# Performance work log

Measured on AMD Instinct MI355X. Metric: run time of the kernel, lower is better.

Reference implementation:

```python
import jax, jax.numpy as jnp
import numpy as np

B, N, D, H, E = 8, 2048, 128, 256, 524288
EPS = 1e-5

def setup_inputs() -> dict:
    key = jax.random.key(0)
    ks = jax.random.split(key, 16)
    def lin(k, fan_in, shape):
        b = 1.0 / np.sqrt(fan_in)
        return jax.random.uniform(k, shape, jnp.float32, -b, b)
    return {
        'x': jax.random.normal(ks[0], (B, N, 3), jnp.float32),
        'h': jax.random.normal(ks[1], (B, N, D), jnp.float32),
        'edge_indices': jax.random.randint(ks[2], (2, E), 0, B * N, jnp.int64),
        'batch_size': B,
        # filter_net: Linear(1,H) -> SiLU -> Linear(H,D)   (weights stored [in,out])
        'W1': lin(ks[3], 1, (1, H)), 'b1': lin(ks[4], 1, (H,)),
        'W2': lin(ks[5], H, (H, D)), 'b2': lin(ks[6], H, (D,)),
        # update_net: Linear(2D,H) -> LayerNorm(H) -> SiLU -> Linear(H,D)
        'W3': lin(ks[7], 2 * D, (2 * D, H)), 'b3': lin(ks[8], 2 * D, (H,)),
        'gamma': jnp.ones((H,), jnp.float32), 'beta': jnp.zeros((H,), jnp.float32),
        'W4': lin(ks[9], H, (H, D)), 'b4': lin(ks[10], H, (D,)),
    }

def reference(x, h, edge_indices, batch_size, W1, b1, W2, b2, W3, b3, gamma, beta, W4, b4):
    Bn, Nn, Dn = h.shape
    row, col = edge_indices[0], edge_indices[1]
    br, nr = row // Nn, row % Nn
    bc, nc = col // Nn, col % Nn
    x_row = x[br, nr]            # [E,3] gather
    x_col = x[bc, nc]            # [E,3]
    h_col = h[bc, nc]            # [E,D]
    diff = x_row - x_col
    dist = jnp.sqrt(jnp.sum(diff * diff, axis=-1, keepdims=True))  # [E,1]
    # distance-conditioned edge filter MLP
    edge_filters = jax.nn.silu(dist @ W1 + b1) @ W2 + b2           # [E,D]
    messages = h_col * edge_filters                                 # [E,D]
    # scatter-mean into B*N nodes (single-pass sum + count, clamp_min(1))
    n_tot = Bn * Nn
    sums = jax.ops.segment_sum(messages, row, num_segments=n_tot)
    counts = jax.ops.segment_sum(jnp.ones_like(row, dtype=messages.dtype), row, num_segments=n_tot)
    agg = (sums / jnp.maximum(counts, 1.0)[:, None]).reshape(Bn, Nn, Dn)
    # update MLP with LayerNorm
    u = jnp.concatenate([h, agg], axis=-1) @ W3 + b3               # [B,N,H]
    mu = jnp.mean(u, axis=-1, keepdims=True)
    var = jnp.mean((u - mu) ** 2, axis=-1, keepdims=True)
    un = (u - mu) * jax.lax.rsqrt(var + EPS) * gamma + beta
    return jax.nn.silu(un) @ W4 + b4                                # [B,N,D]
```

## Files before the change

### kernel.cpp

```cpp
#include <hip/hip_runtime.h>
#include <hip/hip_fp16.h>
#include <math.h>

#define BN_NODES 16384
#define DIM 128
#define HID 256
#define TK 4096
#define TRANGE 32.0f
#define TSTEP (TRANGE / (float)TK)
#define TINV  ((float)TK / TRANGE)
#define LN_EPS 1e-5f
#define EPB 4096
#define NBINS 1024
#define CAPB 768

typedef _Float16 f16x8 __attribute__((ext_vector_type(8)));
typedef __attribute__((ext_vector_type(4))) float f32x4;
typedef __attribute__((ext_vector_type(2))) float floatx2;
typedef __attribute__((ext_vector_type(8))) unsigned short ushort8v;

__device__ __forceinline__ unsigned short f2h(float f) {
    _Float16 h = (_Float16)f;
    return *(unsigned short*)&h;
}
__device__ __forceinline__ __half2 u2h2(unsigned int u) {
    union { unsigned int u; __half2 h; } c; c.u = u; return c.h;
}

__device__ __forceinline__ void edge_acc(unsigned int rec, int dd,
        const unsigned char* __restrict__ xq,
        const unsigned short* __restrict__ Tb, float& a0, float& a1) {
    int c = (int)((rec >> 12) & 0x3FFFu);
    int k = (int)(rec & 0xFFFu);
    unsigned short hq = *(const unsigned short*)&xq[c * DIM + dd];
    unsigned int tv = *(const unsigned int*)&Tb[k * DIM + dd];
    floatx2 hf = __builtin_amdgcn_cvt_pk_f32_fp8((int)hq, false);
    __half2 th = u2h2(tv);
    a0 = fmaf(hf[0], __low2float(th), a0);
    a1 = fmaf(hf[1], __high2float(th), a1);
}

__device__ __forceinline__ void node_tail(const unsigned int* lrec, int from, int to,
        int dd, const unsigned char* __restrict__ xq,
        const unsigned short* __restrict__ Tb, float& a0, float& a1) {
    int i = from;
    for (; i + 4 <= to; i += 4) {
        unsigned int e0 = lrec[i], e1 = lrec[i + 1], e2 = lrec[i + 2], e3 = lrec[i + 3];
        edge_acc(e0, dd, xq, Tb, a0, a1);
        edge_acc(e1, dd, xq, Tb, a0, a1);
        edge_acc(e2, dd, xq, Tb, a0, a1);
        edge_acc(e3, dd, xq, Tb, a0, a1);
    }
    for (; i < to; ++i) edge_acc(lrec[i], dd, xq, Tb, a0, a1);
}

__global__ __launch_bounds__(256) void prep_kernel(
        const float* __restrict__ W1, const float* __restrict__ b1,
        const float* __restrict__ W2, const float* __restrict__ b2,
        const float* __restrict__ W3, const float* __restrict__ W4,
        const float* __restrict__ h, const int* __restrict__ ei,
        const float* __restrict__ x,
        unsigned short* __restrict__ Tb, unsigned short* __restrict__ w3t,
        unsigned short* __restrict__ w4t, unsigned short* __restrict__ xh,
        unsigned char* __restrict__ xq, int* __restrict__ bin_cursor,
        unsigned int* __restrict__ staging, int nE) {
    __shared__ float smem[8 * 256 + 8 * 128];
    int bid = blockIdx.x, t = threadIdx.x;
    if (bid < 512) {
        float* a    = smem;
        float* part = smem + 8 * 256;
        int k0 = bid * 8;
        float w1 = W1[t], bb = b1[t];
#pragma unroll
        for (int k = 0; k < 8; ++k) {
            float dist = ((float)(k0 + k) + 0.5f) * TSTEP;
            float z = dist * w1 + bb;
            a[k * 256 + t] = z / (1.0f + expf(-z));
        }
        __syncthreads();
        int hg = t >> 7, d = t & 127;
        float acc[8] = {0.f,0.f,0.f,0.f,0.f,0.f,0.f,0.f};
        for (int hh = 0; hh < 128; ++hh) {
            int hidx = hg * 128 + hh;
            float w = W2[hidx * DIM + d];
#pragma unroll
            for (int k = 0; k < 8; ++k) acc[k] += a[k * 256 + hidx] * w;
        }
        if (hg == 1) {
#pragma unroll
            for (int k = 0; k < 8; ++k) part[k * 128 + d] = acc[k];
        }
        __syncthreads();
        if (hg == 0) {
            float bd = b2[d];
#pragma unroll
            for (int k = 0; k < 8; ++k)
                Tb[(k0 + k) * DIM + d] = f2h(acc[k] + part[k * 128 + d] + bd);
        }
    } else if (bid < 576) {
        float* s = smem;
        int tid = bid - 512, tr = tid >> 3, tc = tid & 7;
        int lr = t >> 5, lc = t & 31;
#pragma unroll
        for (int rep = 0; rep < 4; ++rep) {
            int k = tr * 32 + rep * 8 + lr, n = tc * 32 + lc;
            s[lc * 33 + rep * 8 + lr] = W3[k * 256 + n];
        }
        __syncthreads();
#pragma unroll
        for (int rep = 0; rep < 4; ++rep) {
            int n = tc * 32 + rep * 8 + lr, k = tr * 32 + lc;
            w3t[n * 256 + k] = f2h(s[(rep * 8 + lr) * 33 + lc]);
        }
    } else if (bid < 608) {
        float* s = smem;
        int tid = bid - 576, tr = tid >> 2, tc = tid & 3;
        int lr = t >> 5, lc = t & 31;
#pragma unroll
        for (int rep = 0; rep < 4; ++rep) {
            int k = tr * 32 + rep * 8 + lr, n = tc * 32 + lc;
            s[lc * 33 + rep * 8 + lr] = W4[k * 128 + n];
        }
        __syncthreads();
#pragma unroll
        for (int rep = 0; rep < 4; ++rep) {
            int n = tc * 32 + rep * 8 + lr, k = tr * 32 + lc;
            w4t[n * 256 + k] = f2h(s[(rep * 8 + lr) * 33 + lc]);
        }
    } else if (bid < 1632) {
        int i0 = (bid - 608) * 2048 + t * 8;
        float4 v0 = *(const float4*)&h[i0];
        float4 v1 = *(const float4*)&h[i0 + 4];
        ushort8v o;
        o[0] = f2h(v0.x); o[1] = f2h(v0.y); o[2] = f2h(v0.z); o[3] = f2h(v0.w);
        o[4] = f2h(v1.x); o[5] = f2h(v1.y); o[6] = f2h(v1.z); o[7] = f2h(v1.w);
        *(ushort8v*)&xh[i0] = o;
        unsigned int q0 = 0, q1 = 0;
        q0 = __builtin_amdgcn_cvt_pk_fp8_f32(v0.x, v0.y, q0, false);
        q0 = __builtin_amdgcn_cvt_pk_fp8_f32(v0.z, v0.w, q0, true);
        q1 = __builtin_amdgcn_cvt_pk_fp8_f32(v1.x, v1.y, q1, false);
        q1 = __builtin_amdgcn_cvt_pk_fp8_f32(v1.z, v1.w, q1, true);
        uint2 qq; qq.x = q0; qq.y = q1;
        *(uint2*)&xq[i0] = qq;
    } else {
        __shared__ int cnt[NBINS];
        __shared__ int pre[NBINS];
        __shared__ int gba[NBINS];
        __shared__ int sc[256];
        __shared__ unsigned int rec[EPB];
        int e0 = (bid - 1632) * EPB;
        int m = min(EPB, nE - e0);
        if (m < 0) m = 0;
#pragma unroll
        for (int j = 0; j < 4; ++j) cnt[j * 256 + t] = 0;
        __syncthreads();
        unsigned int code[16];
        int rk[16], bn[16];
#pragma unroll
        for (int j = 0; j < 16; ++j) {
            int idx = j * 256 + t;
            rk[j] = -1; bn[j] = 0; code[j] = 0;
            if (idx < m) {
                int e = e0 + idx;
                int r = ei[e], c = ei[nE + e];
                code[j] = ((unsigned int)r << 14) | (unsigned int)c;
                bn[j] = r >> 4;
                rk[j] = atomicAdd(&cnt[bn[j]], 1);
            }
        }
        __syncthreads();
        int c4[4], s4 = 0;
#pragma unroll
        for (int j = 0; j < 4; ++j) { c4[j] = cnt[t * 4 + j]; s4 += c4[j]; }
        sc[t] = s4;
        __syncthreads();
        for (int off = 1; off < 256; off <<= 1) {
            int v = (t >= off) ? sc[t - off] : 0;
            __syncthreads();
            sc[t] += v;
            __syncthreads();
        }
        int run = sc[t] - s4;
#pragma unroll
        for (int j = 0; j < 4; ++j) {
            int b = t * 4 + j;
            pre[b] = run; run += c4[j];
            gba[b] = atomicAdd(&bin_cursor[b], c4[j]);
        }
        __syncthreads();
#pragma unroll
        for (int j = 0; j < 16; ++j)
            if (rk[j] >= 0) rec[pre[bn[j]] + rk[j]] = code[j];
        __syncthreads();
        for (int i = t; i < m; i += 256) {
            unsigned int cd = rec[i];
            int b = (int)(cd >> 18);
            int r = (int)(cd >> 14);
            int c = (int)(cd & 0x3FFFu);
            float dx = x[r * 3 + 0] - x[c * 3 + 0];
            float dy = x[r * 3 + 1] - x[c * 3 + 1];
            float dz = x[r * 3 + 2] - x[c * 3 + 2];
            float u = sqrtf(dx * dx + dy * dy + dz * dz) * TINV;
            int k = min((int)u, TK - 1);
            unsigned int o = ((unsigned int)(r & 15) << 26)
                           | ((unsigned int)c << 12) | (unsigned int)k;
            int off = gba[b] + (i - pre[b]);
            if (off < CAPB) staging[b * CAPB + off] = o;
        }
    }
}

__global__ __launch_bounds__(512, 8) void mega_kernel(
        const unsigned int* __restrict__ staging, const int* __restrict__ bin_cursor,
        const unsigned short* __restrict__ Tb, const unsigned char* __restrict__ xq,
        const unsigned short* __restrict__ xh, const unsigned short* __restrict__ w3t,
        const float* __restrict__ b3, const float* __restrict__ gamma,
        const float* __restrict__ beta, const unsigned short* __restrict__ w4t,
        const float* __restrict__ b4, float* __restrict__ out) {
    __shared__ unsigned int lrec[CAPB];
    __shared__ int cnt16[16];
    __shared__ int pref[17];
    __shared__ int cur[16];
    __shared__ __align__(16) unsigned short aggh[16][136];
    __shared__ __align__(16) unsigned short a_lds[16][264];
    __shared__ float part_s[8][16], part_q[8][16];
    __shared__ float tot_mu[16], tot_rs[16];

    int t = threadIdx.x;
    int bin = blockIdx.x;
    int n0 = bin * 16;
    if (t < 16) cnt16[t] = 0;
    __syncthreads();
    int total = min(bin_cursor[bin], CAPB);
    long base = (long)bin * CAPB;

    unsigned int sr0 = 0, sr1 = 0;
    int have0 = (t < total), have1 = (t + 512 < total);
    if (have0) { sr0 = staging[base + t];       atomicAdd(&cnt16[sr0 >> 26], 1); }
    if (have1) { sr1 = staging[base + t + 512]; atomicAdd(&cnt16[sr1 >> 26], 1); }
    __syncthreads();
    if (t < 16) {
        int c = cnt16[t];
        int s = c;
#pragma unroll
        for (int off = 1; off < 16; off <<= 1) {
            int v = __shfl_up(s, off, 16);
            if (t >= off) s += v;
        }
        pref[t + 1] = s;
        cur[t] = s - c;
        if (t == 0) pref[0] = 0;
    }
    __syncthreads();

    if (have0) { int pos = atomicAdd(&cur[sr0 >> 26], 1); lrec[pos] = sr0; }
    if (have1) { int pos = atomicAdd(&cur[sr1 >> 26], 1); lrec[pos] = sr1; }
    __syncthreads();

    int wid = t >> 6, lane = t & 63, dd = lane * 2;

    {
        int j0 = wid * 2, j1 = j0 + 1;
        int off0 = pref[j0], len0 = pref[j0 + 1] - off0;
        int off1 = pref[j1], len1 = pref[j1 + 1] - off1;
        float a0x = 0.f, a0y = 0.f, a1x = 0.f, a1y = 0.f;
        int minl = min(len0, len1);
        int i = 0;
        for (; i + 8 <= minl; i += 8) {
#pragma unroll
            for (int u = 0; u < 8; ++u) {
                edge_acc(lrec[off0 + i + u], dd, xq, Tb, a0x, a0y);
                edge_acc(lrec[off1 + i + u], dd, xq, Tb, a1x, a1y);
            }
        }
        node_tail(lrec, off0 + i, off0 + len0, dd, xq, Tb, a0x, a0y);
        node_tail(lrec, off1 + i, off1 + len1, dd, xq, Tb, a1x, a1y);
        float inv0 = 1.0f / (float)max(len0, 1);
        float inv1 = 1.0f / (float)max(len1, 1);
        unsigned int p0 = (unsigned int)f2h(a0x * inv0) | ((unsigned int)f2h(a0y * inv0) << 16);
        unsigned int p1 = (unsigned int)f2h(a1x * inv1) | ((unsigned int)f2h(a1y * inv1) << 16);
        *(unsigned int*)&aggh[j0][dd] = p0;
        *(unsigned int*)&aggh[j1][dd] = p1;
    }
    __syncthreads();

    int wv = wid, q = lane >> 4, l15 = lane & 15;
    f32x4 acc[2];
    acc[0] = (f32x4){0.f, 0.f, 0.f, 0.f};
    acc[1] = (f32x4){0.f, 0.f, 0.f, 0.f};
    for (int kc = 0; kc < 8; ++kc) {
        f16x8 a;
        if (kc < 4) a = *(const f16x8*)&xh[(n0 + l15) * DIM + kc * 32 + q * 8];
        else        a = *(const f16x8*)&aggh[l15][(kc - 4) * 32 + q * 8];
#pragma unroll
        for (int nt = 0; nt < 2; ++nt) {
            f16x8 b = *(const f16x8*)&w3t[(wv * 32 + nt * 16 + l15) * 256 + kc * 32 + q * 8];
            acc[nt] = __builtin_amdgcn_mfma_f32_16x16x32_f16(a, b, acc[nt], 0, 0, 0);
        }
    }

    float b3v[2], gv[2], bvv[2];
#pragma unroll
    for (int nt = 0; nt < 2; ++nt) {
        int col = wv * 32 + nt * 16 + l15;
        b3v[nt] = b3[col]; gv[nt] = gamma[col]; bvv[nt] = beta[col];
    }
    {
        float s_[4], q_[4];
#pragma unroll
        for (int reg = 0; reg < 4; ++reg) {
            float su = 0.f, sq = 0.f;
#pragma unroll
            for (int nt = 0; nt < 2; ++nt) {
                float v = acc[nt][reg] + b3v[nt];
                acc[nt][reg] = v;
                su += v; sq += v * v;
            }
            s_[reg] = su; q_[reg] = sq;
        }
#pragma unroll
        for (int off = 1; off < 16; off <<= 1) {
#pragma unroll
            for (int reg = 0; reg < 4; ++reg) {
                s_[reg] += __shfl_xor(s_[reg], off, 64);
                q_[reg] += __shfl_xor(q_[reg], off, 64);
            }
        }
        if (l15 == 0) {
#pragma unroll
            for (int reg = 0; reg < 4; ++reg) {
                int r = q * 4 + reg;
                part_s[wv][r] = s_[reg];
                part_q[wv][r] = q_[reg];
            }
        }
    }
    __syncthreads();
    if (t < 16) {
        float st = 0.f, qt = 0.f;
#pragma unroll
        for (int w = 0; w < 8; ++w) { st += part_s[w][t]; qt += part_q[w][t]; }
        float mu = st * (1.0f / 256.0f);
        float var = qt * (1.0f / 256.0f) - mu * mu;
        tot_mu[t] = mu;
        tot_rs[t] = rsqrtf(var + LN_EPS);
    }
    __syncthreads();

#pragma unroll
    for (int reg = 0; reg < 4; ++reg) {
        int r = q * 4 + reg;
        float mu = tot_mu[r], rs = tot_rs[r];
#pragma unroll
        for (int nt = 0; nt < 2; ++nt) {
            float un = (acc[nt][reg] - mu) * rs * gv[nt] + bvv[nt];
            float act = un / (1.0f + expf(-un));
            a_lds[r][wv * 32 + nt * 16 + l15] = f2h(act);
        }
    }
    __syncthreads();

    f32x4 acc2 = (f32x4){0.f, 0.f, 0.f, 0.f};
    int col2 = wv * 16 + l15;
    for (int kc = 0; kc < 8; ++kc) {
        f16x8 a = *(const f16x8*)&a_lds[l15][kc * 32 + q * 8];
        f16x8 b = *(const f16x8*)&w4t[col2 * 256 + kc * 32 + q * 8];
        acc2 = __builtin_amdgcn_mfma_f32_16x16x32_f16(a, b, acc2, 0, 0, 0);
    }
    float b4v = b4[col2];
#pragma unroll
    for (int reg = 0; reg < 4; ++reg) {
        int node = n0 + q * 4 + reg;
        out[node * DIM + col2] = acc2[reg] + b4v;
    }
}

extern "C" void kernel_launch(void* const* d_in, const int* in_sizes, int n_in,
                              void* d_out, int out_size, void* d_ws, size_t ws_size,
                              hipStream_t stream) {
    const float* x     = (const float*)d_in[0];
    const float* h     = (const float*)d_in[1];
    const int*   ei    = (const int*)d_in[2];
    const float* W1    = (const float*)d_in[4];
    const float* b1    = (const float*)d_in[5];
    const float* W2    = (const float*)d_in[6];
    const float* b2    = (const float*)d_in[7];
    const float* W3    = (const float*)d_in[8];
    const float* b3    = (const float*)d_in[9];
    const float* gamma = (const float*)d_in[10];
    const float* beta  = (const float*)d_in[11];
    const float* W4    = (const float*)d_in[12];
    const float* b4    = (const float*)d_in[13];
    float* out = (float*)d_out;
    int nE = in_sizes[2] / 2;

    char* ws = (char*)d_ws;
    unsigned short* Tb   = (unsigned short*)ws; ws += (size_t)TK * DIM * 2;
    unsigned short* w3t  = (unsigned short*)ws; ws += (size_t)HID * HID * 2;
    unsigned short* w4t  = (unsigned short*)ws; ws += (size_t)DIM * HID * 2;
    unsigned short* xh   = (unsigned short*)ws; ws += (size_t)BN_NODES * DIM * 2;
    unsigned char*  xq   = (unsigned char*)ws;  ws += (size_t)BN_NODES * DIM;
    int* bin_cursor = (int*)ws;                 ws += (size_t)NBINS * 4;
    unsigned int* staging = (unsigned int*)ws;  ws += (size_t)NBINS * CAPB * 4;

    int binBlocks = (nE + EPB - 1) / EPB;
    hipMemsetAsync(bin_cursor, 0, (size_t)NBINS * 4, stream);
    prep_kernel<<<1632 + binBlocks, 256, 0, stream>>>(W1, b1, W2, b2, W3, W4, h, ei, x,
                                                      Tb, w3t, w4t, xh, xq,
                                                      bin_cursor, staging, nE);
    mega_kernel<<<NBINS, 512, 0, stream>>>(staging, bin_cursor, Tb, xq, xh,
                                           w3t, b3, gamma, beta, w4t, b4, out);
}
```

Baseline: 161.5 us.

## Quantize edge filter table to scaled FP8 and split each wave across two nodes

The distance-bucketed filter table moves from fp16 to fp8, with a fixed scale of 16 to keep small values representable, and the scale is divided out at the mean. The edge-gather loop is reorganized so each half-wave handles one node, with every lane loading 4 bytes covering 4 feature channels from both the fp8 h and fp8 table, instead of every lane handling 2 channels for two nodes. This halves table bytes per edge and cuts load instructions per edge. The cost is extra precision loss in the filter values and divergence when the two nodes in a wave have different edge counts.

```diff
diff --git a/kernel.cpp b/kernel.cpp
--- a/kernel.cpp
+++ b/kernel.cpp
@@ -9,6 +9,7 @@
 #define TRANGE 32.0f
 #define TSTEP (TRANGE / (float)TK)
 #define TINV  ((float)TK / TRANGE)
+#define TSCALE 16.0f
 #define LN_EPS 1e-5f
 #define EPB 4096
 #define NBINS 1024
@@ -22,36 +23,6 @@
 __device__ __forceinline__ unsigned short f2h(float f) {
     _Float16 h = (_Float16)f;
     return *(unsigned short*)&h;
-}
-__device__ __forceinline__ __half2 u2h2(unsigned int u) {
-    union { unsigned int u; __half2 h; } c; c.u = u; return c.h;
-}
-
-__device__ __forceinline__ void edge_acc(unsigned int rec, int dd,
-        const unsigned char* __restrict__ xq,
-        const unsigned short* __restrict__ Tb, float& a0, float& a1) {
-    int c = (int)((rec >> 12) & 0x3FFFu);
-    int k = (int)(rec & 0xFFFu);
-    unsigned short hq = *(const unsigned short*)&xq[c * DIM + dd];
-    unsigned int tv = *(const unsigned int*)&Tb[k * DIM + dd];
-    floatx2 hf = __builtin_amdgcn_cvt_pk_f32_fp8((int)hq, false);
-    __half2 th = u2h2(tv);
-    a0 = fmaf(hf[0], __low2float(th), a0);
-    a1 = fmaf(hf[1], __high2float(th), a1);
-}
-
-__device__ __forceinline__ void node_tail(const unsigned int* lrec, int from, int to,
-        int dd, const unsigned char* __restrict__ xq,
-        const unsigned short* __restrict__ Tb, float& a0, float& a1) {
-    int i = from;
-    for (; i + 4 <= to; i += 4) {
-        unsigned int e0 = lrec[i], e1 = lrec[i + 1], e2 = lrec[i + 2], e3 = lrec[i + 3];
-        edge_acc(e0, dd, xq, Tb, a0, a1);
-        edge_acc(e1, dd, xq, Tb, a0, a1);
-        edge_acc(e2, dd, xq, Tb, a0, a1);
-        edge_acc(e3, dd, xq, Tb, a0, a1);
-    }
-    for (; i < to; ++i) edge_acc(lrec[i], dd, xq, Tb, a0, a1);
 }
 
 __global__ __launch_bounds__(256) void prep_kernel(
@@ -60,7 +31,7 @@
         const float* __restrict__ W3, const float* __restrict__ W4,
         const float* __restrict__ h, const int* __restrict__ ei,
         const float* __restrict__ x,
-        unsigned short* __restrict__ Tb, unsigned short* __restrict__ w3t,
+        unsigned char* __restrict__ Tb8, unsigned short* __restrict__ w3t,
         unsigned short* __restrict__ w4t, unsigned short* __restrict__ xh,
         unsigned char* __restrict__ xq, int* __restrict__ bin_cursor,
         unsigned int* __restrict__ staging, int nE) {
@@ -94,8 +65,11 @@
         if (hg == 0) {
             float bd = b2[d];
 #pragma unroll
-            for (int k = 0; k < 8; ++k)
-                Tb[(k0 + k) * DIM + d] = f2h(acc[k] + part[k * 128 + d] + bd);
+            for (int k = 0; k < 8; ++k) {
+                float v = (acc[k] + part[k * 128 + d] + bd) * TSCALE;
+                unsigned int q = __builtin_amdgcn_cvt_pk_fp8_f32(v, v, 0, false);
+                Tb8[(k0 + k) * DIM + d] = (unsigned char)(q & 0xFFu);
+            }
         }
     } else if (bid < 576) {
         float* s = smem;
@@ -212,7 +186,7 @@
 
 __global__ __launch_bounds__(512, 8) void mega_kernel(
         const unsigned int* __restrict__ staging, const int* __restrict__ bin_cursor,
-        const unsigned short* __restrict__ Tb, const unsigned char* __restrict__ xq,
+        const unsigned char* __restrict__ Tb8, const unsigned char* __restrict__ xq,
         const unsigned short* __restrict__ xh, const unsigned short* __restrict__ w3t,
         const float* __restrict__ b3, const float* __restrict__ gamma,
         const float* __restrict__ beta, const unsigned short* __restrict__ w4t,
@@ -257,30 +231,59 @@
     if (have1) { int pos = atomicAdd(&cur[sr1 >> 26], 1); lrec[pos] = sr1; }
     __syncthreads();
 
-    int wid = t >> 6, lane = t & 63, dd = lane * 2;
+    int wid = t >> 6, lane = t & 63;
 
     {
-        int j0 = wid * 2, j1 = j0 + 1;
-        int off0 = pref[j0], len0 = pref[j0 + 1] - off0;
-        int off1 = pref[j1], len1 = pref[j1 + 1] - off1;
-        float a0x = 0.f, a0y = 0.f, a1x = 0.f, a1y = 0.f;
-        int minl = min(len0, len1);
+        int half = lane >> 5, l32 = lane & 31, dd4 = l32 * 4;
+        int j = wid * 2 + half;
+        int offj = pref[j], lenj = pref[j + 1] - offj;
+        int len0 = pref[wid * 2 + 1] - pref[wid * 2];
+        int len1 = pref[wid * 2 + 2] - pref[wid * 2 + 1];
+        int lenmax = max(len0, len1);
+        float a0 = 0.f, a1 = 0.f, a2 = 0.f, a3 = 0.f;
         int i = 0;
-        for (; i + 8 <= minl; i += 8) {
-#pragma unroll
-            for (int u = 0; u < 8; ++u) {
-                edge_acc(lrec[off0 + i + u], dd, xq, Tb, a0x, a0y);
-                edge_acc(lrec[off1 + i + u], dd, xq, Tb, a1x, a1y);
-            }
-        }
-        node_tail(lrec, off0 + i, off0 + len0, dd, xq, Tb, a0x, a0y);
-        node_tail(lrec, off1 + i, off1 + len1, dd, xq, Tb, a1x, a1y);
-        float inv0 = 1.0f / (float)max(len0, 1);
-        float inv1 = 1.0f / (float)max(len1, 1);
-        unsigned int p0 = (unsigned int)f2h(a0x * inv0) | ((unsigned int)f2h(a0y * inv0) << 16);
-        unsigned int p1 = (unsigned int)f2h(a1x * inv1) | ((unsigned int)f2h(a1y * inv1) << 16);
-        *(unsigned int*)&aggh[j0][dd] = p0;
-        *(unsigned int*)&aggh[j1][dd] = p1;
+        for (; i + 4 <= lenmax; i += 4) {
+#pragma unroll
+            for (int u = 0; u < 4; ++u) {
+                if (i + u < lenj) {
+                    unsigned int rec = lrec[offj + i + u];
+                    int c = (int)((rec >> 12) & 0x3FFFu);
+                    int k = (int)(rec & 0xFFFu);
+                    unsigned int hx = *(const unsigned int*)&xq[c * DIM + dd4];
+                    unsigned int tv = *(const unsigned int*)&Tb8[k * DIM + dd4];
+                    floatx2 h01 = __builtin_amdgcn_cvt_pk_f32_fp8((int)hx, false);
+                    floatx2 h23 = __builtin_amdgcn_cvt_pk_f32_fp8((int)hx, true);
+                    floatx2 t01 = __builtin_amdgcn_cvt_pk_f32_fp8((int)tv, false);
+                    floatx2 t23 = __builtin_amdgcn_cvt_pk_f32_fp8((int)tv, true);
+                    a0 = fmaf(h01[0], t01[0], a0);
+                    a1 = fmaf(h01[1], t01[1], a1);
+                    a2 = fmaf(h23[0], t23[0], a2);
+                    a3 = fmaf(h23[1], t23[1], a3);
+                }
+            }
+        }
+        for (; i < lenmax; ++i) {
+            if (i < lenj) {
+                unsigned int rec = lrec[offj + i];
+                int c = (int)((rec >> 12) & 0x3FFFu);
+                int k = (int)(rec & 0xFFFu);
+                unsigned int hx = *(const unsigned int*)&xq[c * DIM + dd4];
+                unsigned int tv = *(const unsigned int*)&Tb8[k * DIM + dd4];
+                floatx2 h01 = __builtin_amdgcn_cvt_pk_f32_fp8((int)hx, false);
+                floatx2 h23 = __builtin_amdgcn_cvt_pk_f32_fp8((int)hx, true);
+                floatx2 t01 = __builtin_amdgcn_cvt_pk_f32_fp8((int)tv, false);
+                floatx2 t23 = __builtin_amdgcn_cvt_pk_f32_fp8((int)tv, true);
+                a0 = fmaf(h01[0], t01[0], a0);
+                a1 = fmaf(h01[1], t01[1], a1);
+                a2 = fmaf(h23[0], t23[0], a2);
+                a3 = fmaf(h23[1], t23[1], a3);
+            }
+        }
+        float inv = 1.0f / ((float)max(lenj, 1) * TSCALE);
+        uint2 pp;
+        pp.x = (unsigned int)f2h(a0 * inv) | ((unsigned int)f2h(a1 * inv) << 16);
+        pp.y = (unsigned int)f2h(a2 * inv) | ((unsigned int)f2h(a3 * inv) << 16);
+        *(uint2*)&aggh[j][dd4] = pp;
     }
     __syncthreads();
 
@@ -395,7 +398,7 @@
     int nE = in_sizes[2] / 2;
 
     char* ws = (char*)d_ws;
-    unsigned short* Tb   = (unsigned short*)ws; ws += (size_t)TK * DIM * 2;
+    unsigned char*  Tb8  = (unsigned char*)ws;  ws += (size_t)TK * DIM;
     unsigned short* w3t  = (unsigned short*)ws; ws += (size_t)HID * HID * 2;
     unsigned short* w4t  = (unsigned short*)ws; ws += (size_t)DIM * HID * 2;
     unsigned short* xh   = (unsigned short*)ws; ws += (size_t)BN_NODES * DIM * 2;
@@ -406,8 +409,8 @@
     int binBlocks = (nE + EPB - 1) / EPB;
     hipMemsetAsync(bin_cursor, 0, (size_t)NBINS * 4, stream);
     prep_kernel<<<1632 + binBlocks, 256, 0, stream>>>(W1, b1, W2, b2, W3, W4, h, ei, x,
-                                                      Tb, w3t, w4t, xh, xq,
+                                                      Tb8, w3t, w4t, xh, xq,
                                                       bin_cursor, staging, nE);
-    mega_kernel<<<NBINS, 512, 0, stream>>>(staging, bin_cursor, Tb, xq, xh,
+    mega_kernel<<<NBINS, 512, 0, stream>>>(staging, bin_cursor, Tb8, xq, xh,
                                            w3t, b3, gamma, beta, w4t, b4, out);
 }
```

Measured after the change: 169.9 us. 5.2% more time.
